# Kernel tuning notes

Hardware: AMD Instinct MI355X
Metric: run time of the kernel (lower is better)

The kernel has to match this reference:

```python
import jax, jax.numpy as jnp
import numpy as np

H = 32          # total heads
K = 8           # active heads per token
D = 128         # head_dim = embed_dim // active_heads
E = 1024        # embed_dim
S = 1024        # seq_len
MAX_SEQ = 8192
BASE = 10000.0
SCALE = D ** -0.5
LB_W = 0.01
ENT_W = 0.01


def _rope(v, cos, sin):
    # v: (T, D); cos/sin: (T, D)
    v1, v2 = v[:, : D // 2], v[:, D // 2:]
    rot = jnp.concatenate([-v2, v1], axis=-1)
    return v * cos + rot * sin


def setup_inputs() -> dict:
    key = jax.random.key(0)
    ks = jax.random.split(key, 6)
    x = jax.random.normal(ks[0], (1, S, E), jnp.float32)
    Wq = jax.random.normal(ks[1], (E, H * D), jnp.float32) * 0.02
    Wk = jax.random.normal(ks[2], (E, H * D), jnp.float32) * 0.02
    Wv = jax.random.normal(ks[3], (E, H * D), jnp.float32) * 0.02
    Wr = jax.random.normal(ks[4], (E, H), jnp.float32) * 0.02
    Wo = jax.random.normal(ks[5], (K * D, E), jnp.float32) * 0.02
    head_counts = jnp.zeros((1, H), jnp.int32)
    return {"x": x, "Wq": Wq, "Wk": Wk, "Wv": Wv, "Wr": Wr, "Wo": Wo,
            "head_counts": head_counts}


def reference(x, Wq, Wk, Wv, Wr, Wo, head_counts):
    # ---- routing (eval mode: no gumbel noise) ----
    logits = x @ Wr                                   # (1, S, H)
    soft_probs = jax.nn.softmax(logits, axis=-1)
    top_logits, head_idx = jax.lax.top_k(logits, K)   # (1, S, K)
    head_w = jax.nn.softmax(top_logits, axis=-1)      # (1, S, K)

    # ---- aux loss ----
    primary = head_idx[..., 0]                        # (1, S)
    one_hot_p = jax.nn.one_hot(primary, H, dtype=jnp.float32)
    f = one_hot_p.mean(axis=1)                        # (1, H)
    p = soft_probs.mean(axis=1)                       # (1, H)
    balance = H * (f * p).sum(axis=-1).mean()
    entropy = -(soft_probs * jnp.log(soft_probs + 1e-8)).sum(axis=-1)
    entropy_loss = -entropy.mean()
    z_loss = (jax.nn.logsumexp(logits, axis=-1) ** 2).mean() * 0.01
    aux_loss = LB_W * balance + ENT_W * entropy_loss + z_loss

    # ---- projections + per-token gather of selected heads ----
    q_all = (x @ Wq).reshape(1, S, H, D)
    k_all = (x @ Wk).reshape(1, S, H, D)
    v_all = (x @ Wv).reshape(1, S, H, D)
    gidx = head_idx[..., None]                        # (1, S, K, 1)
    q = jnp.take_along_axis(q_all, gidx, axis=2)[0].reshape(S * K, D)
    k = jnp.take_along_axis(k_all, gidx, axis=2)[0].reshape(S * K, D)
    v = jnp.take_along_axis(v_all, gidx, axis=2)[0].reshape(S * K, D)

    heads_flat = head_idx[0].reshape(S * K)           # (T,)

    # rank of each dispatched token within its head (exclusive prefix count)
    oh = jax.nn.one_hot(heads_flat, H, dtype=jnp.int32)   # (T, H)
    excl = jnp.cumsum(oh, axis=0) - oh
    rank = jnp.take_along_axis(excl, heads_flat[:, None], axis=1)[:, 0]
    positions = rank + head_counts[0, heads_flat]
    positions = jnp.clip(positions, 0, MAX_SEQ - 1)

    # ---- per-head RoPE with per-head position counters ----
    inv_freq = 1.0 / (BASE ** (jnp.arange(0, D, 2, dtype=jnp.float32) / D))
    freqs = positions.astype(jnp.float32)[:, None] * inv_freq[None, :]
    emb = jnp.concatenate([freqs, freqs], axis=-1)    # (T, D)
    cos, sin = jnp.cos(emb), jnp.sin(emb)
    q = _rope(q, cos, sin)
    k = _rope(k, cos, sin)

    # ---- block-diagonal-causal attention (same head, earlier dispatch order) ----
    idx = jnp.arange(S * K)
    mask = (heads_flat[:, None] == heads_flat[None, :]) & (idx[None, :] <= idx[:, None])
    scores = (q @ k.T) * SCALE                        # (T, T)
    scores = jnp.where(mask, scores, jnp.float32(-1e30))
    attn = jax.nn.softmax(scores, axis=-1)
    out = attn @ v                                    # (T, D)

    # ---- combine with routing weights + output projection ----
    out = out.reshape(S, K, D) * head_w[0][..., None]
    out = out.reshape(S, K * D) @ Wo                  # (S, E)
    output = out[None]                                # (1, S, E)

    updated_counts = head_counts + oh.sum(axis=0)[None]
    return output, updated_counts, aux_loss
```

## Files before the change

### kernel.cpp

```cpp
#include <hip/hip_runtime.h>
#include <math.h>

#define S 1024
#define E 1024
#define H 32
#define KSEL 8
#define D 128
#define HD 4096
#define SK 8192
#define MAXL 1024
#define CAP 9216
#define ATTN_SCALE 0.08838834764831845f
#define SSTR 36
#define PSTR 40

#define NROUTER 256
#define NTAB 512

typedef _Float16 half8 __attribute__((ext_vector_type(8)));
typedef _Float16 half4 __attribute__((ext_vector_type(4)));
typedef float floatx16 __attribute__((ext_vector_type(16)));
typedef float f4 __attribute__((ext_vector_type(4)));

#define GLOAD_LDS16(gsrc, ldst) \
    __builtin_amdgcn_global_load_lds( \
        (const __attribute__((address_space(1))) void*)(gsrc), \
        (__attribute__((address_space(3))) void*)(ldst), 16, 0, 0)

__device__ __forceinline__ void head_prefix(const int* __restrict__ hlen, int h,
                                            int lane, int& len, int& hb, int& lenp)
{
    int hl = (lane < 32) ? hlen[lane] : 0;
    int hp = (hl + 31) & ~31;
    int pref = hp;
    #pragma unroll
    for (int off = 1; off < 32; off <<= 1) {
        int t = __shfl_up(pref, off, 64);
        if (lane >= off) pref += t;
    }
    int excl = pref - hp;
    hb   = __shfl(excl, h, 64);
    len  = __shfl(hl, h, 64);
    lenp = (len + 31) & ~31;
}

__global__ __launch_bounds__(256) void conv_kernel(
    const float* __restrict__ Wq, const float* __restrict__ Wk,
    const float* __restrict__ Wv, const float* __restrict__ Wo,
    _Float16* __restrict__ Wqkt, _Float16* __restrict__ Wot)
{
    int cb = blockIdx.x, tid = threadIdx.x;
    __shared__ _Float16 tl[128 * 128];
    int z, rem;
    if (cb < 768) { z = cb >> 8; rem = cb & 255; }
    else          { z = 3;       rem = cb - 768; }
    const float* W = (z == 0) ? Wq : (z == 1) ? Wk : (z == 2) ? Wv : Wo;
    _Float16* T = (z < 3) ? (Wqkt + (size_t)z * HD * E) : Wot;
    int C = (z < 3) ? HD : 1024;
    int nc = C >> 7;
    int c0 = (rem % nc) * 128;
    int r0 = (rem / nc) * 128;
    #pragma unroll
    for (int p = 0; p < 16; ++p) {
        int idx = p * 256 + tid;
        int rr = idx >> 5, cg = (idx & 31) * 4;
        f4 v = *(const f4*)&W[(size_t)(r0 + rr) * C + c0 + cg];
        half4 o;
        o.x = (_Float16)v.x; o.y = (_Float16)v.y;
        o.z = (_Float16)v.z; o.w = (_Float16)v.w;
        int sc = cg ^ (((rr >> 3) & 7) << 2);
        *(half4*)&tl[rr * 128 + sc] = o;
    }
    __syncthreads();
    #pragma unroll
    for (int p = 0; p < 8; ++p) {
        int chunk = p * 256 + tid;
        int cc = chunk >> 4, ch = chunk & 15;
        int cidx = cc ^ ((ch & 7) << 2);
        half8 o;
        #pragma unroll
        for (int j = 0; j < 8; ++j)
            o[j] = tl[(ch * 8 + j) * 128 + cidx];
        *(half8*)&T[(size_t)(c0 + cc) * 1024 + r0 + ch * 8] = o;
    }
}

__global__ __launch_bounds__(256) void router_tab_kernel(
    const float* __restrict__ x, const float* __restrict__ Wr,
    int* __restrict__ head_idx, float* __restrict__ head_w,
    float* __restrict__ pbuf, float* __restrict__ entz,
    _Float16* __restrict__ xh, float2* __restrict__ tab)
{
    int bid = blockIdx.x, tid = threadIdx.x;
    if (bid >= NROUTER) {
        int base = (bid - NROUTER) * 1024;
        #pragma unroll
        for (int j = 0; j < 4; ++j) {
            int idx = base + j * 256 + tid;
            int p = idx >> 6, d2 = idx & 63;
            float inv = exp2f((float)d2 * -0.20762050f);
            float ang = (float)p * inv;
            float sn, cs;
            sincosf(ang, &sn, &cs);
            tab[idx] = make_float2(cs, sn);
        }
        return;
    }
    int s = bid * 4 + (tid >> 6);
    int lane = tid & 63;
    int h = lane & 31, half = lane >> 5;
    const float* xr = x + (size_t)s * E + half * 512;
    const float* wr = Wr + (size_t)(half * 512) * H + h;
    float a0 = 0.f, a1 = 0.f, a2 = 0.f, a3 = 0.f;
    #pragma unroll 4
    for (int e = 0; e < 512; e += 4) {
        a0 += xr[e]     * wr[e * H];
        a1 += xr[e + 1] * wr[(e + 1) * H];
        a2 += xr[e + 2] * wr[(e + 2) * H];
        a3 += xr[e + 3] * wr[(e + 3) * H];
    }
    float acc = (a0 + a1) + (a2 + a3);
    acc += __shfl_xor(acc, 32, 64);
    float logit = acc;
    float m = logit;
    #pragma unroll
    for (int off = 16; off; off >>= 1) m = fmaxf(m, __shfl_xor(m, off, 64));
    float ex = expf(logit - m);
    float Z = ex;
    #pragma unroll
    for (int off = 16; off; off >>= 1) Z += __shfl_xor(Z, off, 64);
    float p = ex / Z;
    float es = p * logf(p + 1e-8f);
    #pragma unroll
    for (int off = 16; off; off >>= 1) es += __shfl_xor(es, off, 64);
    float lse = m + logf(Z);
    float lv = logit;
    float tv[KSEL]; int ti[KSEL];
    #pragma unroll
    for (int j = 0; j < KSEL; ++j) {
        float bv = lv; int bi = h;
        #pragma unroll
        for (int off = 16; off; off >>= 1) {
            float ov = __shfl_xor(bv, off, 64);
            int oi = __shfl_xor(bi, off, 64);
            if (ov > bv || (ov == bv && oi < bi)) { bv = ov; bi = oi; }
        }
        tv[j] = bv; ti[j] = bi;
        if (h == bi) lv = -INFINITY;
    }
    float Z2 = 0.f;
    #pragma unroll
    for (int j = 0; j < KSEL; ++j) Z2 += expf(tv[j] - tv[0]);
    if (lane < 32) pbuf[s * 32 + lane] = p;
    if (lane == 0) {
        entz[s * 2]     = es;
        entz[s * 2 + 1] = lse * lse;
        #pragma unroll
        for (int j = 0; j < KSEL; ++j) {
            head_idx[s * KSEL + j] = ti[j];
            head_w[s * KSEL + j]   = expf(tv[j] - tv[0]) / Z2;
        }
    }
    const float* xrow = x + (size_t)s * E;
    _Float16* xhrow = xh + (size_t)s * E;
    #pragma unroll
    for (int t = 0; t < 4; ++t) {
        int e = t * 256 + lane * 4;
        f4 v = *(const f4*)&xrow[e];
        half4 o;
        o.x = (_Float16)v.x; o.y = (_Float16)v.y; o.z = (_Float16)v.z; o.w = (_Float16)v.w;
        *(half4*)&xhrow[e] = o;
    }
}

__global__ __launch_bounds__(256) void scan_aux_kernel(
    const int* __restrict__ head_idx, const int* __restrict__ head_counts,
    int* __restrict__ order, int* __restrict__ hlen, float* __restrict__ out_counts,
    const float* __restrict__ pbuf, const float* __restrict__ entz,
    float* __restrict__ out_aux)
{
    int bid = blockIdx.x, tid = threadIdx.x;
    if (bid == H) {
        int hh = tid & 31, grp = tid >> 5;
        __shared__ float red[256], red2[256];
        __shared__ float psum[32];
        __shared__ int hist[32];
        if (tid < 32) hist[tid] = 0;
        float ps = 0.f;
        for (int s = grp; s < S; s += 8) ps += pbuf[s * 32 + hh];
        red[tid] = ps;
        float es = 0.f, zs = 0.f;
        for (int s = tid; s < S; s += 256) { es += entz[s * 2]; zs += entz[s * 2 + 1]; }
        red2[tid] = es;
        __syncthreads();
        if (grp == 0) {
            float v = 0.f;
            #pragma unroll
            for (int j = 0; j < 8; ++j) v += red[j * 32 + hh];
            psum[hh] = v;
        }
        __syncthreads();
        red[tid] = zs;
        for (int s = tid; s < S; s += 256)
            atomicAdd(&hist[head_idx[s * KSEL]], 1);
        __syncthreads();
        for (int stp = 128; stp; stp >>= 1) {
            if (tid < stp) { red[tid] += red[tid + stp]; red2[tid] += red2[tid + stp]; }
            __syncthreads();
        }
        if (tid == 0) {
            float bal = 0.f;
            for (int j = 0; j < H; ++j)
                bal += ((float)hist[j] / (float)S) * (psum[j] / (float)S);
            bal *= (float)H;
            float ent_loss = red2[0] / (float)S;
            float z = red[0] / (float)S * 0.01f;
            out_aux[0] = 0.01f * bal + 0.01f * ent_loss + z;
        }
        return;
    }
    int h = bid;
    int wave = tid >> 6, lane = tid & 63;
    __shared__ int wtot[4][4];
    int base = 0;
    int hc = head_counts[h];
    int v0 = head_idx[tid],       v1 = head_idx[256 + tid];
    int v2 = head_idx[512 + tid], v3 = head_idx[768 + tid];
    unsigned long long lt = (1ull << lane) - 1ull;
    for (int c0 = 0; c0 < SK; c0 += 1024) {
        int n0 = 0, n1 = 0, n2 = 0, n3 = 0;
        if (c0 + 1024 < SK) {
            n0 = head_idx[c0 + 1024 + tid]; n1 = head_idx[c0 + 1280 + tid];
            n2 = head_idx[c0 + 1536 + tid]; n3 = head_idx[c0 + 1792 + tid];
        }
        bool p0 = (v0 == h), p1 = (v1 == h), p2 = (v2 == h), p3 = (v3 == h);
        unsigned long long m0 = __ballot(p0), m1 = __ballot(p1);
        unsigned long long m2 = __ballot(p2), m3 = __ballot(p3);
        int w0 = __popcll(m0 & lt), w1 = __popcll(m1 & lt);
        int w2 = __popcll(m2 & lt), w3 = __popcll(m3 & lt);
        if (lane == 0) {
            wtot[0][wave] = __popcll(m0); wtot[1][wave] = __popcll(m1);
            wtot[2][wave] = __popcll(m2); wtot[3][wave] = __popcll(m3);
        }
        __syncthreads();
        int pw[4], T[4];
        #pragma unroll
        for (int i = 0; i < 4; ++i) {
            int pre = 0, tot = 0;
            #pragma unroll
            for (int w = 0; w < 4; ++w) {
                int tv = wtot[i][w];
                if (w < wave) pre += tv;
                tot += tv;
            }
            pw[i] = pre; T[i] = tot;
        }
        if (p0) order[h * MAXL + base + pw[0] + w0] = c0 + tid;
        if (p1) order[h * MAXL + base + T[0] + pw[1] + w1] = c0 + 256 + tid;
        if (p2) order[h * MAXL + base + T[0] + T[1] + pw[2] + w2] = c0 + 512 + tid;
        if (p3) order[h * MAXL + base + T[0] + T[1] + T[2] + pw[3] + w3] = c0 + 768 + tid;
        base += T[0] + T[1] + T[2] + T[3];
        __syncthreads();
        v0 = n0; v1 = n1; v2 = n2; v3 = n3;
    }
    if (tid == 0) {
        hlen[h] = base;
        out_counts[h] = (float)(hc + base);
    }
}

__global__ __launch_bounds__(256) void qkv_mfma(
    const _Float16* __restrict__ xh, const _Float16* __restrict__ Wt,
    const int* __restrict__ order, const int* __restrict__ hlen,
    const int* __restrict__ head_counts, const float2* __restrict__ tab,
    _Float16* __restrict__ qh, _Float16* __restrict__ kh, _Float16* __restrict__ vT)
{
    int xid = blockIdx.x;
    int qkv = xid >> 5, h = xid & 31;
    int rt = blockIdx.y;
    int tid = threadIdx.x, wave = tid >> 6, lane = tid & 63;
    int len, hb, lenp;
    head_prefix(hlen, h, lane, len, hb, lenp);
    int row0 = rt * 64;
    if (row0 >= len) return;
    int wm = wave >> 1, wn = wave & 1;
    int l32 = lane & 31, g = lane >> 5;

    __shared__ _Float16 Bs[2][128 * 64];

    int arow_g = row0 + wm * 32 + l32;
    int tok = (arow_g < len) ? (order[h * MAXL + arow_g] >> 3) : 0;
    const _Float16* aptr = xh + (size_t)tok * E;
    const _Float16* Wb = Wt + (size_t)((qkv * H + h) * D) * E;

    auto stageB = [&](int buf, int k0) {
        #pragma unroll
        for (int it = 0; it < 4; ++it) {
            int f = it * 256 + tid;
            int row = f >> 3, c = f & 7;
            int sc = c ^ (row & 7);
            const _Float16* src = Wb + (size_t)row * E + k0 + sc * 8;
            GLOAD_LDS16(src, &Bs[buf][f * 8]);
        }
    };

    floatx16 acc[2] = {};
    half8 a_cur[4], a_nxt[4];
    #pragma unroll
    for (int ks = 0; ks < 4; ++ks)
        a_cur[ks] = *(const half8*)(aptr + ks * 16 + g * 8);

    auto compute = [&](int buf, half8* a) {
        #pragma unroll
        for (int ks = 0; ks < 4; ++ks) {
            int wchunk = ks * 2 + g;
            #pragma unroll
            for (int nf = 0; nf < 2; ++nf) {
                int brow = wn * 64 + nf * 32 + l32;
                half8 bf = *(const half8*)&Bs[buf][brow * 64 + (wchunk ^ (brow & 7)) * 8];
                acc[nf] = __builtin_amdgcn_mfma_f32_32x32x16_f16(a[ks], bf, acc[nf], 0, 0, 0);
            }
        }
    };

    stageB(0, 0);
    __syncthreads();
    int buf = 0;
    for (int k0 = 64; k0 < E; k0 += 64) {
        stageB(buf ^ 1, k0);
        #pragma unroll
        for (int ks = 0; ks < 4; ++ks)
            a_nxt[ks] = *(const half8*)(aptr + k0 + ks * 16 + g * 8);
        compute(buf, a_cur);
        __syncthreads();
        buf ^= 1;
        #pragma unroll
        for (int ks = 0; ks < 4; ++ks) a_cur[ks] = a_nxt[ks];
    }
    compute(buf, a_cur);

    if (qkv < 2) {
        _Float16* dst = (qkv == 0) ? qh : kh;
        float* scr = (float*)&Bs[0][0];
        __syncthreads();
        #pragma unroll
        for (int nf = 0; nf < 2; ++nf) {
            int col = wn * 64 + nf * 32 + l32;
            #pragma unroll
            for (int reg = 0; reg < 16; ++reg) {
                int rl = wm * 32 + (reg & 3) + 8 * (reg >> 2) + 4 * g;
                scr[rl * 128 + col] = acc[nf][reg];
            }
        }
        __syncthreads();
        int hc = head_counts[h];
        #pragma unroll
        for (int pass = 0; pass < 16; ++pass) {
            int idx = pass * 256 + tid;
            int r = idx >> 6, d2 = idx & 63;
            int slot = row0 + r;
            if (slot < len) {
                float v1 = scr[r * 128 + d2], v2 = scr[r * 128 + 64 + d2];
                int p = slot + hc;
                p = p < 0 ? 0 : (p > 8191 ? 8191 : p);
                float2 tt = tab[p * 64 + d2];
                _Float16* dp = dst + ((size_t)hb + slot) * D;
                dp[d2]      = (_Float16)(v1 * tt.x - v2 * tt.y);
                dp[d2 + 64] = (_Float16)(v2 * tt.x + v1 * tt.y);
            }
        }
    } else {
        #pragma unroll
        for (int nf = 0; nf < 2; ++nf) {
            int col = wn * 64 + nf * 32 + l32;
            #pragma unroll
            for (int q4 = 0; q4 < 4; ++q4) {
                int slot0 = row0 + wm * 32 + 8 * q4 + 4 * g;
                _Float16* vp = vT + (size_t)hb * D + (size_t)col * lenp + slot0;
                if (slot0 + 3 < len) {
                    half4 o;
                    o.x = (_Float16)acc[nf][q4 * 4 + 0];
                    o.y = (_Float16)acc[nf][q4 * 4 + 1];
                    o.z = (_Float16)acc[nf][q4 * 4 + 2];
                    o.w = (_Float16)acc[nf][q4 * 4 + 3];
                    *(half4*)vp = o;
                } else {
                    #pragma unroll
                    for (int r2 = 0; r2 < 4; ++r2) {
                        int sl = slot0 + r2;
                        if (sl < len) vp[r2] = (_Float16)acc[nf][q4 * 4 + r2];
                        else if (sl < lenp) vp[r2] = (_Float16)0.f;
                    }
                }
            }
        }
    }
}

__global__ __launch_bounds__(128) void attn_mfma(
    const _Float16* __restrict__ qh, const _Float16* __restrict__ kh,
    const _Float16* __restrict__ vT,
    const int* __restrict__ order, const int* __restrict__ hlen,
    const float* __restrict__ head_w, _Float16* __restrict__ ao)
{
    int h = blockIdx.x >> 5, qt = blockIdx.x & 31;
    int tid = threadIdx.x;
    int w = tid >> 6, lane = tid & 63;
    int len, hb, lenp;
    head_prefix(hlen, h, lane, len, hb, lenp);
    int row0 = qt * 32;
    if (row0 >= len) return;
    int l32 = lane & 31, g = lane >> 5;
    int srow = lane >> 1, shalf = lane & 1;

    __shared__ float Sld[2][32 * SSTR];
    __shared__ _Float16 Pld[2][32 * PSTR];
    __shared__ float alphaLd[2][32];
    __shared__ float mlLd[32][4];
    __shared__ float facLd[32][3];
    __shared__ int flatLd[32];
    __shared__ float Obuf[32][128];

    if (tid < 32) {
        int r = row0 + tid;
        flatLd[tid] = (r < len) ? order[h * MAXL + r] : -1;
    }

    const _Float16* qrow = qh + ((size_t)hb + row0 + l32) * D;
    half8 qf[8];
    #pragma unroll
    for (int t = 0; t < 8; ++t) qf[t] = *(const half8*)(qrow + t * 16 + g * 8);

    floatx16 O[4] = {};
    float m_run = -INFINITY, l_run = 0.f;

    if (w <= qt) {
        half8 kf[8], kfn[8], vv[8];
        {
            const _Float16* krow = kh + ((size_t)hb + w * 32 + l32) * D;
            #pragma unroll
            for (int t = 0; t < 8; ++t) kf[t] = *(const half8*)(krow + t * 16 + g * 8);
        }
        for (int kt = w; kt <= qt; kt += 2) {
            int col0 = kt * 32;
            floatx16 Sc = {};
            #pragma unroll
            for (int t = 0; t < 8; ++t)
                Sc = __builtin_amdgcn_mfma_f32_32x32x16_f16(qf[t], kf[t], Sc, 0, 0, 0);
            #pragma unroll
            for (int nt = 0; nt < 4; ++nt) {
                const _Float16* vp = vT + (size_t)hb * D + (size_t)(nt * 32 + l32) * lenp + col0;
                vv[nt * 2]     = *(const half8*)(vp + g * 8);
                vv[nt * 2 + 1] = *(const half8*)(vp + 16 + g * 8);
            }
            if (kt + 2 <= qt) {
                const _Float16* krow = kh + ((size_t)hb + col0 + 64 + l32) * D;
                #pragma unroll
                for (int t = 0; t < 8; ++t) kfn[t] = *(const half8*)(krow + t * 16 + g * 8);
            }
            bool diag = (kt == qt);
            #pragma unroll
            for (int reg = 0; reg < 16; ++reg) {
                int row = (reg & 3) + 8 * (reg >> 2) + 4 * g;
                float s = Sc[reg] * ATTN_SCALE;
                if (diag && l32 > row) s = -1e30f;
                Sld[w][row * SSTR + l32] = s;
            }
            __builtin_amdgcn_wave_barrier();
            const float* sp = &Sld[w][srow * SSTR + shalf * 16];
            float va[16];
            *(f4*)(va)      = *(const f4*)(sp);
            *(f4*)(va + 4)  = *(const f4*)(sp + 4);
            *(f4*)(va + 8)  = *(const f4*)(sp + 8);
            *(f4*)(va + 12) = *(const f4*)(sp + 12);
            float mt_ = va[0];
            #pragma unroll
            for (int j = 1; j < 16; ++j) mt_ = fmaxf(mt_, va[j]);
            mt_ = fmaxf(mt_, __shfl_xor(mt_, 1, 64));
            float m_new = fmaxf(m_run, mt_);
            float alpha = __expf(m_run - m_new);
            float p[16], tsum = 0.f;
            #pragma unroll
            for (int j = 0; j < 16; ++j) { p[j] = __expf(va[j] - m_new); tsum += p[j]; }
            tsum += __shfl_xor(tsum, 1, 64);
            l_run = l_run * alpha + tsum;
            m_run = m_new;
            half8 ph0, ph1;
            #pragma unroll
            for (int j = 0; j < 8; ++j) { ph0[j] = (_Float16)p[j]; ph1[j] = (_Float16)p[j + 8]; }
            *(half8*)&Pld[w][srow * PSTR + shalf * 16]     = ph0;
            *(half8*)&Pld[w][srow * PSTR + shalf * 16 + 8] = ph1;
            if (shalf == 0) alphaLd[w][srow] = alpha;
            __builtin_amdgcn_wave_barrier();
            f4 al[4];
            #pragma unroll
            for (int qq = 0; qq < 4; ++qq) al[qq] = *(const f4*)&alphaLd[w][4 * g + 8 * qq];
            #pragma unroll
            for (int reg = 0; reg < 16; ++reg) {
                float av = al[reg >> 2][reg & 3];
                O[0][reg] *= av; O[1][reg] *= av; O[2][reg] *= av; O[3][reg] *= av;
            }
            half8 pf0 = *(const half8*)&Pld[w][l32 * PSTR + g * 8];
            half8 pf1 = *(const half8*)&Pld[w][l32 * PSTR + 16 + g * 8];
            #pragma unroll
            for (int nt = 0; nt < 4; ++nt) {
                O[nt] = __builtin_amdgcn_mfma_f32_32x32x16_f16(pf0, vv[nt * 2],     O[nt], 0, 0, 0);
                O[nt] = __builtin_amdgcn_mfma_f32_32x32x16_f16(pf1, vv[nt * 2 + 1], O[nt], 0, 0, 0);
            }
            __builtin_amdgcn_wave_barrier();
            #pragma unroll
            for (int t = 0; t < 8; ++t) kf[t] = kfn[t];
        }
    }
    if (shalf == 0) { mlLd[srow][w * 2] = m_run; mlLd[srow][w * 2 + 1] = l_run; }
    __syncthreads();
    if (tid < 32) {
        float m0 = mlLd[tid][0], l0 = mlLd[tid][1];
        float m1 = mlLd[tid][2], l1 = mlLd[tid][3];
        float ms = fmaxf(m0, m1);
        float f0 = __expf(m0 - ms), f1 = __expf(m1 - ms);
        float lt = f0 * l0 + f1 * l1;
        int flat = flatLd[tid];
        float hw = (flat >= 0) ? head_w[flat] : 0.f;
        facLd[tid][0] = f1;
        facLd[tid][1] = hw / lt;
        facLd[tid][2] = f0;
    }
    __syncthreads();
    if (w == 1) {
        #pragma unroll
        for (int nt = 0; nt < 4; ++nt) {
            int col = nt * 32 + l32;
            #pragma unroll
            for (int reg = 0; reg < 16; ++reg) {
                int row = (reg & 3) + 8 * (reg >> 2) + 4 * g;
                Obuf[row][col] = O[nt][reg] * facLd[row][0];
            }
        }
    }
    __syncthreads();
    if (w == 0) {
        #pragma unroll
        for (int nt = 0; nt < 4; ++nt) {
            int col = nt * 32 + l32;
            #pragma unroll
            for (int reg = 0; reg < 16; ++reg) {
                int row = (reg & 3) + 8 * (reg >> 2) + 4 * g;
                int flat = flatLd[row];
                if (flat >= 0) {
                    float val = (O[nt][reg] * facLd[row][2] + Obuf[row][col]) * facLd[row][1];
                    ao[(size_t)flat * D + col] = (_Float16)val;
                }
            }
        }
    }
}

__global__ __launch_bounds__(256) void out_mfma(
    const _Float16* __restrict__ A, const _Float16* __restrict__ Bt,
    float* __restrict__ C)
{
    int n0 = blockIdx.x * 64, m0 = blockIdx.y * 64;
    int tid = threadIdx.x, wave = tid >> 6, lane = tid & 63;
    int wm = wave >> 1, wn = wave & 1;
    int l32 = lane & 31, g = lane >> 5;

    __shared__ _Float16 Bs[2][64 * 64];

    const _Float16* aptr = A + (size_t)(m0 + wm * 32 + l32) * 1024;

    auto stageB = [&](int buf, int k0) {
        #pragma unroll
        for (int it = 0; it < 2; ++it) {
            int f = it * 256 + tid;
            int row = f >> 3, c = f & 7;
            int sc = c ^ (row & 7);
            GLOAD_LDS16(Bt + (size_t)(n0 + row) * 1024 + k0 + sc * 8, &Bs[buf][f * 8]);
        }
    };

    floatx16 acc = {};
    int brow = wn * 32 + l32;
    half8 a_cur[4], a_nxt[4];
    #pragma unroll
    for (int ks = 0; ks < 4; ++ks)
        a_cur[ks] = *(const half8*)(aptr + ks * 16 + g * 8);

    auto compute = [&](int buf, half8* a) {
        #pragma unroll
        for (int ks = 0; ks < 4; ++ks) {
            int wchunk = ks * 2 + g;
            half8 bf = *(const half8*)&Bs[buf][brow * 64 + (wchunk ^ (brow & 7)) * 8];
            acc = __builtin_amdgcn_mfma_f32_32x32x16_f16(a[ks], bf, acc, 0, 0, 0);
        }
    };

    stageB(0, 0);
    __syncthreads();
    int buf = 0;
    for (int k0 = 64; k0 < 1024; k0 += 64) {
        stageB(buf ^ 1, k0);
        #pragma unroll
        for (int ks = 0; ks < 4; ++ks)
            a_nxt[ks] = *(const half8*)(aptr + k0 + ks * 16 + g * 8);
        compute(buf, a_cur);
        __syncthreads();
        buf ^= 1;
        #pragma unroll
        for (int ks = 0; ks < 4; ++ks) a_cur[ks] = a_nxt[ks];
    }
    compute(buf, a_cur);

    int col = n0 + wn * 32 + l32;
    #pragma unroll
    for (int reg = 0; reg < 16; ++reg) {
        int row = m0 + wm * 32 + (reg & 3) + 8 * (reg >> 2) + 4 * g;
        C[(size_t)row * 1024 + col] = acc[reg];
    }
}

extern "C" void kernel_launch(void* const* d_in, const int* in_sizes, int n_in,
                              void* d_out, int out_size, void* d_ws, size_t ws_size,
                              hipStream_t stream)
{
    const float* x  = (const float*)d_in[0];
    const float* Wq = (const float*)d_in[1];
    const float* Wk = (const float*)d_in[2];
    const float* Wv = (const float*)d_in[3];
    const float* Wr = (const float*)d_in[4];
    const float* Wo = (const float*)d_in[5];
    const int* head_counts = (const int*)d_in[6];
    float* out = (float*)d_out;

    float* head_w = (float*)d_ws;
    float* pbuf   = head_w + SK;
    float* entz   = pbuf + S * 32;
    int* head_idx = (int*)(entz + S * 2);
    int* order    = head_idx + SK;
    int* hlen     = order + H * MAXL;
    _Float16* xh   = (_Float16*)(hlen + 64);
    _Float16* aoh  = xh + (size_t)S * E;
    _Float16* Wqkt = aoh + (size_t)SK * D;
    _Float16* Wot  = Wqkt + (size_t)3 * HD * E;
    _Float16* qh   = Wot + (size_t)1024 * 1024;
    _Float16* kh   = qh + (size_t)CAP * D;
    _Float16* vT   = kh + (size_t)CAP * D;
    float2* tab    = (float2*)(vT + (size_t)CAP * D);

    router_tab_kernel<<<NROUTER + NTAB, 256, 0, stream>>>(
        x, Wr, head_idx, head_w, pbuf, entz, xh, tab);
    conv_kernel<<<832, 256, 0, stream>>>(Wq, Wk, Wv, Wo, Wqkt, Wot);
    scan_aux_kernel<<<33, 256, 0, stream>>>(head_idx, head_counts, order, hlen,
                                            out + (size_t)S * E, pbuf, entz,
                                            out + (size_t)S * E + H);
    qkv_mfma<<<dim3(96, 16), 256, 0, stream>>>(xh, Wqkt, order, hlen, head_counts, tab,
                                               qh, kh, vT);
    attn_mfma<<<H * 32, 128, 0, stream>>>(qh, kh, vT, order, hlen, head_w, aoh);
    out_mfma<<<dim3(16, 16), 256, 0, stream>>>(aoh, Wot, out);
}
```

Measured before the change: 226.8 us.

## Fuse weight conversion into router kernel; double QKV row tile and attention block size

Folds the weight transpose/convert kernel into the router/RoPE-table kernel so one launch does both. The QKV projection now processes 128 rows per block with two accumulator sets, so each staged weight tile is reused twice. The attention kernel packs two 32-row query tiles into a 256-thread block. This cuts launch count and weight-tile reloads, but raises register use and can leave more waves idle for short heads.

Result: slower. 232.2 us (+2.4%).

```diff
diff --git a/kernel.cpp b/kernel.cpp
--- a/kernel.cpp
+++ b/kernel.cpp
@@ -15,6 +15,7 @@
 #define PSTR 40
 
 #define NROUTER 256
+#define NCONV 832
 #define NTAB 512
 
 typedef _Float16 half8 __attribute__((ext_vector_type(8)));
@@ -44,56 +45,19 @@
     lenp = (len + 31) & ~31;
 }
 
-__global__ __launch_bounds__(256) void conv_kernel(
-    const float* __restrict__ Wq, const float* __restrict__ Wk,
-    const float* __restrict__ Wv, const float* __restrict__ Wo,
-    _Float16* __restrict__ Wqkt, _Float16* __restrict__ Wot)
-{
-    int cb = blockIdx.x, tid = threadIdx.x;
-    __shared__ _Float16 tl[128 * 128];
-    int z, rem;
-    if (cb < 768) { z = cb >> 8; rem = cb & 255; }
-    else          { z = 3;       rem = cb - 768; }
-    const float* W = (z == 0) ? Wq : (z == 1) ? Wk : (z == 2) ? Wv : Wo;
-    _Float16* T = (z < 3) ? (Wqkt + (size_t)z * HD * E) : Wot;
-    int C = (z < 3) ? HD : 1024;
-    int nc = C >> 7;
-    int c0 = (rem % nc) * 128;
-    int r0 = (rem / nc) * 128;
-    #pragma unroll
-    for (int p = 0; p < 16; ++p) {
-        int idx = p * 256 + tid;
-        int rr = idx >> 5, cg = (idx & 31) * 4;
-        f4 v = *(const f4*)&W[(size_t)(r0 + rr) * C + c0 + cg];
-        half4 o;
-        o.x = (_Float16)v.x; o.y = (_Float16)v.y;
-        o.z = (_Float16)v.z; o.w = (_Float16)v.w;
-        int sc = cg ^ (((rr >> 3) & 7) << 2);
-        *(half4*)&tl[rr * 128 + sc] = o;
-    }
-    __syncthreads();
-    #pragma unroll
-    for (int p = 0; p < 8; ++p) {
-        int chunk = p * 256 + tid;
-        int cc = chunk >> 4, ch = chunk & 15;
-        int cidx = cc ^ ((ch & 7) << 2);
-        half8 o;
-        #pragma unroll
-        for (int j = 0; j < 8; ++j)
-            o[j] = tl[(ch * 8 + j) * 128 + cidx];
-        *(half8*)&T[(size_t)(c0 + cc) * 1024 + r0 + ch * 8] = o;
-    }
-}
-
-__global__ __launch_bounds__(256) void router_tab_kernel(
+__global__ __launch_bounds__(256) void router_conv_kernel(
     const float* __restrict__ x, const float* __restrict__ Wr,
     int* __restrict__ head_idx, float* __restrict__ head_w,
     float* __restrict__ pbuf, float* __restrict__ entz,
-    _Float16* __restrict__ xh, float2* __restrict__ tab)
+    _Float16* __restrict__ xh,
+    const float* __restrict__ Wq, const float* __restrict__ Wk,
+    const float* __restrict__ Wv, const float* __restrict__ Wo,
+    _Float16* __restrict__ Wqkt, _Float16* __restrict__ Wot,
+    float2* __restrict__ tab)
 {
     int bid = blockIdx.x, tid = threadIdx.x;
-    if (bid >= NROUTER) {
-        int base = (bid - NROUTER) * 1024;
+    if (bid >= NROUTER + NCONV) {
+        int base = (bid - NROUTER - NCONV) * 1024;
         #pragma unroll
         for (int j = 0; j < 4; ++j) {
             int idx = base + j * 256 + tid;
@@ -103,6 +67,43 @@
             float sn, cs;
             sincosf(ang, &sn, &cs);
             tab[idx] = make_float2(cs, sn);
+        }
+        return;
+    }
+    if (bid >= NROUTER) {
+        __shared__ _Float16 tl[128 * 128];
+        int cb = bid - NROUTER;
+        int z, rem;
+        if (cb < 768) { z = cb >> 8; rem = cb & 255; }
+        else          { z = 3;       rem = cb - 768; }
+        const float* W = (z == 0) ? Wq : (z == 1) ? Wk : (z == 2) ? Wv : Wo;
+        _Float16* T = (z < 3) ? (Wqkt + (size_t)z * HD * E) : Wot;
+        int C = (z < 3) ? HD : 1024;
+        int nc = C >> 7;
+        int c0 = (rem % nc) * 128;
+        int r0 = (rem / nc) * 128;
+        #pragma unroll
+        for (int p = 0; p < 16; ++p) {
+            int idx = p * 256 + tid;
+            int rr = idx >> 5, cg = (idx & 31) * 4;
+            f4 v = *(const f4*)&W[(size_t)(r0 + rr) * C + c0 + cg];
+            half4 o;
+            o.x = (_Float16)v.x; o.y = (_Float16)v.y;
+            o.z = (_Float16)v.z; o.w = (_Float16)v.w;
+            int sc = cg ^ (((rr >> 3) & 7) << 2);
+            *(half4*)&tl[rr * 128 + sc] = o;
+        }
+        __syncthreads();
+        #pragma unroll
+        for (int p = 0; p < 8; ++p) {
+            int chunk = p * 256 + tid;
+            int cc = chunk >> 4, ch = chunk & 15;
+            int cidx = cc ^ ((ch & 7) << 2);
+            half8 o;
+            #pragma unroll
+            for (int j = 0; j < 8; ++j)
+                o[j] = tl[(ch * 8 + j) * 128 + cidx];
+            *(half8*)&T[(size_t)(c0 + cc) * 1024 + r0 + ch * 8] = o;
         }
         return;
     }
@@ -281,16 +282,21 @@
     int tid = threadIdx.x, wave = tid >> 6, lane = tid & 63;
     int len, hb, lenp;
     head_prefix(hlen, h, lane, len, hb, lenp);
-    int row0 = rt * 64;
+    int row0 = rt * 128;
     if (row0 >= len) return;
+    bool sub1 = (row0 + 64 < len);
     int wm = wave >> 1, wn = wave & 1;
     int l32 = lane & 31, g = lane >> 5;
 
     __shared__ _Float16 Bs[2][128 * 64];
 
-    int arow_g = row0 + wm * 32 + l32;
-    int tok = (arow_g < len) ? (order[h * MAXL + arow_g] >> 3) : 0;
-    const _Float16* aptr = xh + (size_t)tok * E;
+    const _Float16* aptr[2];
+    #pragma unroll
+    for (int rb = 0; rb < 2; ++rb) {
+        int arow_g = row0 + rb * 64 + wm * 32 + l32;
+        int tok = (arow_g < len) ? (order[h * MAXL + arow_g] >> 3) : 0;
+        aptr[rb] = xh + (size_t)tok * E;
+    }
     const _Float16* Wb = Wt + (size_t)((qkv * H + h) * D) * E;
 
     auto stageB = [&](int buf, int k0) {
@@ -304,13 +310,15 @@
         }
     };
 
-    floatx16 acc[2] = {};
-    half8 a_cur[4], a_nxt[4];
-    #pragma unroll
-    for (int ks = 0; ks < 4; ++ks)
-        a_cur[ks] = *(const half8*)(aptr + ks * 16 + g * 8);
-
-    auto compute = [&](int buf, half8* a) {
+    floatx16 acc[2][2] = {};
+    half8 a_cur[2][4], a_nxt[2][4];
+    #pragma unroll
+    for (int rb = 0; rb < 2; ++rb)
+        #pragma unroll
+        for (int ks = 0; ks < 4; ++ks)
+            a_cur[rb][ks] = *(const half8*)(aptr[rb] + ks * 16 + g * 8);
+
+    auto compute = [&](int buf, half8 a[2][4]) {
         #pragma unroll
         for (int ks = 0; ks < 4; ++ks) {
             int wchunk = ks * 2 + g;
@@ -318,7 +326,9 @@
             for (int nf = 0; nf < 2; ++nf) {
                 int brow = wn * 64 + nf * 32 + l32;
                 half8 bf = *(const half8*)&Bs[buf][brow * 64 + (wchunk ^ (brow & 7)) * 8];
-                acc[nf] = __builtin_amdgcn_mfma_f32_32x32x16_f16(a[ks], bf, acc[nf], 0, 0, 0);
+                #pragma unroll
+                for (int rb = 0; rb < 2; ++rb)
+                    acc[rb][nf] = __builtin_amdgcn_mfma_f32_32x32x16_f16(a[rb][ks], bf, acc[rb][nf], 0, 0, 0);
             }
         }
     };
@@ -329,67 +339,78 @@
     for (int k0 = 64; k0 < E; k0 += 64) {
         stageB(buf ^ 1, k0);
         #pragma unroll
-        for (int ks = 0; ks < 4; ++ks)
-            a_nxt[ks] = *(const half8*)(aptr + k0 + ks * 16 + g * 8);
+        for (int rb = 0; rb < 2; ++rb)
+            #pragma unroll
+            for (int ks = 0; ks < 4; ++ks)
+                a_nxt[rb][ks] = *(const half8*)(aptr[rb] + k0 + ks * 16 + g * 8);
         compute(buf, a_cur);
         __syncthreads();
         buf ^= 1;
         #pragma unroll
-        for (int ks = 0; ks < 4; ++ks) a_cur[ks] = a_nxt[ks];
+        for (int rb = 0; rb < 2; ++rb)
+            #pragma unroll
+            for (int ks = 0; ks < 4; ++ks) a_cur[rb][ks] = a_nxt[rb][ks];
     }
     compute(buf, a_cur);
 
     if (qkv < 2) {
         _Float16* dst = (qkv == 0) ? qh : kh;
         float* scr = (float*)&Bs[0][0];
-        __syncthreads();
-        #pragma unroll
-        for (int nf = 0; nf < 2; ++nf) {
-            int col = wn * 64 + nf * 32 + l32;
-            #pragma unroll
-            for (int reg = 0; reg < 16; ++reg) {
-                int rl = wm * 32 + (reg & 3) + 8 * (reg >> 2) + 4 * g;
-                scr[rl * 128 + col] = acc[nf][reg];
-            }
-        }
-        __syncthreads();
         int hc = head_counts[h];
-        #pragma unroll
-        for (int pass = 0; pass < 16; ++pass) {
-            int idx = pass * 256 + tid;
-            int r = idx >> 6, d2 = idx & 63;
-            int slot = row0 + r;
-            if (slot < len) {
-                float v1 = scr[r * 128 + d2], v2 = scr[r * 128 + 64 + d2];
-                int p = slot + hc;
-                p = p < 0 ? 0 : (p > 8191 ? 8191 : p);
-                float2 tt = tab[p * 64 + d2];
-                _Float16* dp = dst + ((size_t)hb + slot) * D;
-                dp[d2]      = (_Float16)(v1 * tt.x - v2 * tt.y);
-                dp[d2 + 64] = (_Float16)(v2 * tt.x + v1 * tt.y);
+        for (int rb = 0; rb < 2; ++rb) {
+            if (rb && !sub1) break;
+            __syncthreads();
+            #pragma unroll
+            for (int nf = 0; nf < 2; ++nf) {
+                int col = wn * 64 + nf * 32 + l32;
+                #pragma unroll
+                for (int reg = 0; reg < 16; ++reg) {
+                    int rl = wm * 32 + (reg & 3) + 8 * (reg >> 2) + 4 * g;
+                    scr[rl * 128 + col] = acc[rb][nf][reg];
+                }
+            }
+            __syncthreads();
+            #pragma unroll
+            for (int pass = 0; pass < 16; ++pass) {
+                int idx = pass * 256 + tid;
+                int r = idx >> 6, d2 = idx & 63;
+                int slot = row0 + rb * 64 + r;
+                if (slot < len) {
+                    float v1 = scr[r * 128 + d2], v2 = scr[r * 128 + 64 + d2];
+                    int p = slot + hc;
+                    p = p < 0 ? 0 : (p > 8191 ? 8191 : p);
+                    float2 tt = tab[p * 64 + d2];
+                    _Float16* dp = dst + ((size_t)hb + slot) * D;
+                    dp[d2]      = (_Float16)(v1 * tt.x - v2 * tt.y);
+                    dp[d2 + 64] = (_Float16)(v2 * tt.x + v1 * tt.y);
+                }
             }
         }
     } else {
         #pragma unroll
-        for (int nf = 0; nf < 2; ++nf) {
-            int col = wn * 64 + nf * 32 + l32;
-            #pragma unroll
-            for (int q4 = 0; q4 < 4; ++q4) {
-                int slot0 = row0 + wm * 32 + 8 * q4 + 4 * g;
-                _Float16* vp = vT + (size_t)hb * D + (size_t)col * lenp + slot0;
-                if (slot0 + 3 < len) {
-                    half4 o;
-                    o.x = (_Float16)acc[nf][q4 * 4 + 0];
-                    o.y = (_Float16)acc[nf][q4 * 4 + 1];
-                    o.z = (_Float16)acc[nf][q4 * 4 + 2];
-                    o.w = (_Float16)acc[nf][q4 * 4 + 3];
-                    *(half4*)vp = o;
-                } else {
-                    #pragma unroll
-                    for (int r2 = 0; r2 < 4; ++r2) {
-                        int sl = slot0 + r2;
-                        if (sl < len) vp[r2] = (_Float16)acc[nf][q4 * 4 + r2];
-                        else if (sl < lenp) vp[r2] = (_Float16)0.f;
+        for (int rb = 0; rb < 2; ++rb) {
+            if (rb && !sub1) break;
+            #pragma unroll
+            for (int nf = 0; nf < 2; ++nf) {
+                int col = wn * 64 + nf * 32 + l32;
+                #pragma unroll
+                for (int q4 = 0; q4 < 4; ++q4) {
+                    int slot0 = row0 + rb * 64 + wm * 32 + 8 * q4 + 4 * g;
+                    _Float16* vp = vT + (size_t)hb * D + (size_t)col * lenp + slot0;
+                    if (slot0 + 3 < len) {
+                        half4 o;
+                        o.x = (_Float16)acc[rb][nf][q4 * 4 + 0];
+                        o.y = (_Float16)acc[rb][nf][q4 * 4 + 1];
+                        o.z = (_Float16)acc[rb][nf][q4 * 4 + 2];
+                        o.w = (_Float16)acc[rb][nf][q4 * 4 + 3];
+                        *(half4*)vp = o;
+                    } else {
+                        #pragma unroll
+                        for (int r2 = 0; r2 < 4; ++r2) {
+                            int sl = slot0 + r2;
+                            if (sl < len) vp[r2] = (_Float16)acc[rb][nf][q4 * 4 + r2];
+                            else if (sl < lenp) vp[r2] = (_Float16)0.f;
+                        }
                     }
                 }
             }
@@ -397,36 +418,41 @@
     }
 }
 
-__global__ __launch_bounds__(128) void attn_mfma(
+__global__ __launch_bounds__(256) void attn_mfma(
     const _Float16* __restrict__ qh, const _Float16* __restrict__ kh,
     const _Float16* __restrict__ vT,
     const int* __restrict__ order, const int* __restrict__ hlen,
     const float* __restrict__ head_w, _Float16* __restrict__ ao)
 {
-    int h = blockIdx.x >> 5, qt = blockIdx.x & 31;
+    int h = blockIdx.x >> 4, qt2 = blockIdx.x & 15;
     int tid = threadIdx.x;
     int w = tid >> 6, lane = tid & 63;
+    int wq = w >> 1, ws = w & 1;
     int len, hb, lenp;
     head_prefix(hlen, h, lane, len, hb, lenp);
-    int row0 = qt * 32;
+    int row0 = qt2 * 64;
     if (row0 >= len) return;
     int l32 = lane & 31, g = lane >> 5;
     int srow = lane >> 1, shalf = lane & 1;
-
-    __shared__ float Sld[2][32 * SSTR];
-    __shared__ _Float16 Pld[2][32 * PSTR];
-    __shared__ float alphaLd[2][32];
-    __shared__ float mlLd[32][4];
-    __shared__ float facLd[32][3];
-    __shared__ int flatLd[32];
-    __shared__ float Obuf[32][128];
-
-    if (tid < 32) {
+    int tq = qt2 * 2 + wq;
+    int qrow0 = row0 + wq * 32;
+    bool qvalid = qrow0 < len;
+    int qrow0c = qvalid ? qrow0 : 0;
+
+    __shared__ float Sld[4][32 * SSTR];
+    __shared__ _Float16 Pld[4][32 * PSTR];
+    __shared__ float alphaLd[4][32];
+    __shared__ float mlLd[64][4];
+    __shared__ float facLd[64][3];
+    __shared__ int flatLd[64];
+    __shared__ float Obuf[64][128];
+
+    if (tid < 64) {
         int r = row0 + tid;
         flatLd[tid] = (r < len) ? order[h * MAXL + r] : -1;
     }
 
-    const _Float16* qrow = qh + ((size_t)hb + row0 + l32) * D;
+    const _Float16* qrow = qh + ((size_t)hb + qrow0c + l32) * D;
     half8 qf[8];
     #pragma unroll
     for (int t = 0; t < 8; ++t) qf[t] = *(const half8*)(qrow + t * 16 + g * 8);
@@ -434,14 +460,14 @@
     floatx16 O[4] = {};
     float m_run = -INFINITY, l_run = 0.f;
 
-    if (w <= qt) {
+    if (qvalid && ws <= tq) {
         half8 kf[8], kfn[8], vv[8];
         {
-            const _Float16* krow = kh + ((size_t)hb + w * 32 + l32) * D;
+            const _Float16* krow = kh + ((size_t)hb + ws * 32 + l32) * D;
             #pragma unroll
             for (int t = 0; t < 8; ++t) kf[t] = *(const half8*)(krow + t * 16 + g * 8);
         }
-        for (int kt = w; kt <= qt; kt += 2) {
+        for (int kt = ws; kt <= tq; kt += 2) {
             int col0 = kt * 32;
             floatx16 Sc = {};
             #pragma unroll
@@ -453,12 +479,12 @@
                 vv[nt * 2]     = *(const half8*)(vp + g * 8);
                 vv[nt * 2 + 1] = *(const half8*)(vp + 16 + g * 8);
             }
-            if (kt + 2 <= qt) {
+            if (kt + 2 <= tq) {
                 const _Float16* krow = kh + ((size_t)hb + col0 + 64 + l32) * D;
                 #pragma unroll
                 for (int t = 0; t < 8; ++t) kfn[t] = *(const half8*)(krow + t * 16 + g * 8);
             }
-            bool diag = (kt == qt);
+            bool diag = (kt == tq);
             #pragma unroll
             for (int reg = 0; reg < 16; ++reg) {
                 int row = (reg & 3) + 8 * (reg >> 2) + 4 * g;
@@ -512,9 +538,9 @@
             for (int t = 0; t < 8; ++t) kf[t] = kfn[t];
         }
     }
-    if (shalf == 0) { mlLd[srow][w * 2] = m_run; mlLd[srow][w * 2 + 1] = l_run; }
+    if (shalf == 0) { mlLd[wq * 32 + srow][ws * 2] = m_run; mlLd[wq * 32 + srow][ws * 2 + 1] = l_run; }
     __syncthreads();
-    if (tid < 32) {
+    if (tid < 64) {
         float m0 = mlLd[tid][0], l0 = mlLd[tid][1];
         float m1 = mlLd[tid][2], l1 = mlLd[tid][3];
         float ms = fmaxf(m0, m1);
@@ -527,25 +553,25 @@
         facLd[tid][2] = f0;
     }
     __syncthreads();
-    if (w == 1) {
+    if (ws == 1) {
         #pragma unroll
         for (int nt = 0; nt < 4; ++nt) {
             int col = nt * 32 + l32;
             #pragma unroll
             for (int reg = 0; reg < 16; ++reg) {
-                int row = (reg & 3) + 8 * (reg >> 2) + 4 * g;
+                int row = wq * 32 + (reg & 3) + 8 * (reg >> 2) + 4 * g;
                 Obuf[row][col] = O[nt][reg] * facLd[row][0];
             }
         }
     }
     __syncthreads();
-    if (w == 0) {
+    if (ws == 0) {
         #pragma unroll
         for (int nt = 0; nt < 4; ++nt) {
             int col = nt * 32 + l32;
             #pragma unroll
             for (int reg = 0; reg < 16; ++reg) {
-                int row = (reg & 3) + 8 * (reg >> 2) + 4 * g;
+                int row = wq * 32 + (reg & 3) + 8 * (reg >> 2) + 4 * g;
                 int flat = flatLd[row];
                 if (flat >= 0) {
                     float val = (O[nt][reg] * facLd[row][2] + Obuf[row][col]) * facLd[row][1];
@@ -647,14 +673,13 @@
     _Float16* vT   = kh + (size_t)CAP * D;
     float2* tab    = (float2*)(vT + (size_t)CAP * D);
 
-    router_tab_kernel<<<NROUTER + NTAB, 256, 0, stream>>>(
-        x, Wr, head_idx, head_w, pbuf, entz, xh, tab);
-    conv_kernel<<<832, 256, 0, stream>>>(Wq, Wk, Wv, Wo, Wqkt, Wot);
+    router_conv_kernel<<<NROUTER + NCONV + NTAB, 256, 0, stream>>>(
+        x, Wr, head_idx, head_w, pbuf, entz, xh, Wq, Wk, Wv, Wo, Wqkt, Wot, tab);
     scan_aux_kernel<<<33, 256, 0, stream>>>(head_idx, head_counts, order, hlen,
                                             out + (size_t)S * E, pbuf, entz,
                                             out + (size_t)S * E + H);
-    qkv_mfma<<<dim3(96, 16), 256, 0, stream>>>(xh, Wqkt, order, hlen, head_counts, tab,
-                                               qh, kh, vT);
-    attn_mfma<<<H * 32, 128, 0, stream>>>(qh, kh, vT, order, hlen, head_w, aoh);
+    qkv_mfma<<<dim3(96, 8), 256, 0, stream>>>(xh, Wqkt, order, hlen, head_counts, tab,
+                                              qh, kh, vT);
+    attn_mfma<<<H * 16, 256, 0, stream>>>(qh, kh, vT, order, hlen, head_w, aoh);
     out_mfma<<<dim3(16, 16), 256, 0, stream>>>(aoh, Wot, out);
 }
```
